# Kernel optimization log

Measured on AMD Instinct MI355X. Metric: run time of the kernel, lower is better.

Reference implementation:

```python
import jax, jax.numpy as jnp
import numpy as np

HEADS = 4
OUT_DIM = 64
NEG_SLOPE = 0.2


def setup_inputs() -> dict:
    key = jax.random.key(0)
    k1, k2, k3, k4 = jax.random.split(key, 4)
    n, in_dim = 4096, 256
    x = jax.random.normal(k1, (n, in_dim), dtype=jnp.float32)
    adj = jax.random.randint(k2, (n, n), 0, 2, dtype=jnp.int32)
    # lin: in_dim -> heads*out_dim (no bias), stored as [in_dim, heads*out_dim]
    W = jax.random.normal(k3, (in_dim, HEADS * OUT_DIM), dtype=jnp.float32) * 0.05
    # att_weight: [heads, 2*out_dim]
    att = jax.random.normal(k4, (HEADS, 2 * OUT_DIM), dtype=jnp.float32) * 0.05
    return {"x": x, "adj": adj, "W": W, "att": att}


def reference(x, adj, W, att):
    n = x.shape[0]
    h = (x @ W).reshape(n, HEADS, OUT_DIM)  # [n, H, D]
    # scores[i,j,h] = att[h] . cat(h_i, h_j) = <h_i, a_src[h]> + <h_j, a_dst[h]>
    a_src, a_dst = att[:, :OUT_DIM], att[:, OUT_DIM:]
    e_src = jnp.einsum('nhd,hd->nh', h, a_src)  # [n, H]
    e_dst = jnp.einsum('nhd,hd->nh', h, a_dst)  # [n, H]
    scores = e_src[:, None, :] + e_dst[None, :, :]  # [n, n, H]
    scores = jax.nn.leaky_relu(scores, negative_slope=NEG_SLOPE)
    mask = (adj > 0)[:, :, None]  # [n, n, 1]
    scores = jnp.where(mask, scores, -jnp.inf)
    alpha = jax.nn.softmax(scores, axis=1)  # softmax over neighbors j
    # h_prime[i,h,d] = sum_j alpha[i,j,h] * h[j,h,d]
    h_prime = jnp.einsum('ijh,jhd->ihd', alpha, h)
    return h_prime.reshape(n, HEADS * OUT_DIM)
```

## Files before the change

### kernel.cpp

```cpp
#include <hip/hip_runtime.h>
#include <hip/hip_bf16.h>

#define HEADS 4
#define ODIM 64
#define HD 256
#define NEG_SLOPE 0.2f
#define SPLITS 4
#define BJ 128

typedef __attribute__((ext_vector_type(8))) short bf16x8;
typedef __attribute__((ext_vector_type(4))) float floatx4;
typedef __attribute__((ext_vector_type(2))) float floatx2;

__global__ __launch_bounds__(256) void pack_xw(const float* __restrict__ x,
                                               const float* __restrict__ W,
                                               const int* __restrict__ adj,
                                               __hip_bfloat16* __restrict__ xh,
                                               __hip_bfloat16* __restrict__ xl,
                                               __hip_bfloat16* __restrict__ wh,
                                               __hip_bfloat16* __restrict__ wl,
                                               unsigned long long* __restrict__ adjP,
                                               int K, int n, int nxb, int nwb) {
    const int b = blockIdx.x;
    const int Kc = K >> 5;
    if (b < nxb) {
        const int g = b * 256 + threadIdx.x;
        const int lane = g & 63, frag = g >> 6;
        const int kc = frag % Kc, mc = frag / Kc;
        const int l16 = lane & 15, q = lane >> 4;
        const float* src = x + (size_t)(mc * 16 + l16) * K + kc * 32 + q * 8;
        const float4 v0 = *(const float4*)src;
        const float4 v1 = *(const float4*)(src + 4);
        const float vv[8] = {v0.x, v0.y, v0.z, v0.w, v1.x, v1.y, v1.z, v1.w};
        union { __hip_bfloat16 b[8]; bf16x8 v; } H, L;
        #pragma unroll
        for (int p = 0; p < 8; ++p) {
            H.b[p] = __float2bfloat16(vv[p]);
            L.b[p] = __float2bfloat16(vv[p] - __bfloat162float(H.b[p]));
        }
        *(bf16x8*)&xh[(size_t)frag * 512 + lane * 8] = H.v;
        *(bf16x8*)&xl[(size_t)frag * 512 + lane * 8] = L.v;
    } else if (b < nxb + nwb) {
        const int g = (b - nxb) * 256 + threadIdx.x;
        const int lane = g & 63, frag = g >> 6;
        const int kc = frag % Kc, nc = frag / Kc;
        const int l16 = lane & 15, q = lane >> 4;
        union { __hip_bfloat16 b[8]; bf16x8 v; } H, L;
        #pragma unroll
        for (int p = 0; p < 8; ++p) {
            const float w = W[(size_t)(kc * 32 + q * 8 + p) * HD + nc * 16 + l16];
            H.b[p] = __float2bfloat16(w);
            L.b[p] = __float2bfloat16(w - __bfloat162float(H.b[p]));
        }
        *(bf16x8*)&wh[(size_t)frag * 512 + lane * 8] = H.v;
        *(bf16x8*)&wl[(size_t)frag * 512 + lane * 8] = L.v;
    } else {
        const int bb = b - nxb - nwb;
        const int wv = threadIdx.x >> 6, ln = threadIdx.x & 63;
        const int gw = bb * 4 + wv;
        const int segs = n >> 6;
        for (int t = gw; t < n * 4; t += 1024) {
            const int row = t >> 2, qq = t & 3;
            const int* ar = adj + (size_t)row * n + (size_t)qq * 16 * 64;
            unsigned long long* dst = adjP + (size_t)row * segs + qq * 16;
            int v[16];
            #pragma unroll
            for (int s = 0; s < 16; ++s) v[s] = ar[s * 64 + ln];
            #pragma unroll
            for (int s = 0; s < 16; ++s) {
                const unsigned long long m = __ballot(v[s] > 0);
                if (ln == 0) dst[s] = m;
            }
        }
    }
}

__global__ __launch_bounds__(128) void gemm_fused(
    const __hip_bfloat16* __restrict__ xh, const __hip_bfloat16* __restrict__ xl,
    const __hip_bfloat16* __restrict__ wh, const __hip_bfloat16* __restrict__ wl,
    const float* __restrict__ att, float2* __restrict__ Es, float2* __restrict__ Ed,
    __hip_bfloat16* __restrict__ hbB, int n, int K) {

    __shared__ __hip_bfloat16 T[64][40];

    const int tid = threadIdx.x, wave = tid >> 6, lane = tid & 63;
    const int q = lane >> 4, l16 = lane & 15;
    const int m0 = blockIdx.x * 32;
    const int head = blockIdx.y;
    const int Kc = K >> 5;
    const int mc = (m0 >> 4) + wave;

    floatx4 acc[4] = {{0.f,0.f,0.f,0.f},{0.f,0.f,0.f,0.f},{0.f,0.f,0.f,0.f},{0.f,0.f,0.f,0.f}};

    const __hip_bfloat16* Axh = xh + (size_t)mc * Kc * 512 + lane * 8;
    const __hip_bfloat16* Axl = xl + (size_t)mc * Kc * 512 + lane * 8;
    const __hip_bfloat16* Bwh = wh + lane * 8;
    const __hip_bfloat16* Bwl = wl + lane * 8;
    #pragma unroll 2
    for (int kc = 0; kc < Kc; ++kc) {
        const bf16x8 ah = *(const bf16x8*)(Axh + (size_t)kc * 512);
        const bf16x8 al = *(const bf16x8*)(Axl + (size_t)kc * 512);
        bf16x8 bh[4], bl[4];
        #pragma unroll
        for (int nt = 0; nt < 4; ++nt) {
            const size_t fo = (size_t)((head * 4 + nt) * Kc + kc) * 512;
            bh[nt] = *(const bf16x8*)(Bwh + fo);
            bl[nt] = *(const bf16x8*)(Bwl + fo);
        }
        #pragma unroll
        for (int nt = 0; nt < 4; ++nt)
            acc[nt] = __builtin_amdgcn_mfma_f32_16x16x32_bf16(ah, bh[nt], acc[nt], 0, 0, 0);
        #pragma unroll
        for (int nt = 0; nt < 4; ++nt)
            acc[nt] = __builtin_amdgcn_mfma_f32_16x16x32_bf16(ah, bl[nt], acc[nt], 0, 0, 0);
        #pragma unroll
        for (int nt = 0; nt < 4; ++nt)
            acc[nt] = __builtin_amdgcn_mfma_f32_16x16x32_bf16(al, bh[nt], acc[nt], 0, 0, 0);
    }

    float as_v[4], ad_v[4];
    #pragma unroll
    for (int nt = 0; nt < 4; ++nt) {
        as_v[nt] = att[head * 2 * ODIM + nt * 16 + l16];
        ad_v[nt] = att[head * 2 * ODIM + ODIM + nt * 16 + l16];
    }
    #pragma unroll
    for (int r = 0; r < 4; ++r) {
        float ps = 0.f, pd = 0.f;
        #pragma unroll
        for (int nt = 0; nt < 4; ++nt) {
            ps = fmaf(acc[nt][r], as_v[nt], ps);
            pd = fmaf(acc[nt][r], ad_v[nt], pd);
        }
        #pragma unroll
        for (int m = 1; m <= 8; m <<= 1) {
            ps += __shfl_xor(ps, m, 64);
            pd += __shfl_xor(pd, m, 64);
        }
        if (l16 == 0) {
            const int i = m0 + wave * 16 + q * 4 + r;
            Es[head * n + i] = make_float2(__expf(ps), __expf(NEG_SLOPE * ps));
            Ed[head * n + i] = make_float2(__expf(pd), __expf(NEG_SLOPE * pd));
        }
    }

    #pragma unroll
    for (int nt = 0; nt < 4; ++nt) {
        union { __hip_bfloat16 b[4]; uint2 u; } pk;
        #pragma unroll
        for (int r = 0; r < 4; ++r) pk.b[r] = __float2bfloat16(acc[nt][r]);
        *(uint2*)&T[nt * 16 + l16][wave * 16 + q * 4] = pk.u;
    }
    __syncthreads();

    #pragma unroll
    for (int ffi = 0; ffi < 2; ++ffi) {
        const int f = wave + ffi * 2;
        const bf16x8 v = *(const bf16x8*)&T[f * 16 + l16][q * 8];
        const size_t frag = ((size_t)head * (n >> 5) + (m0 >> 5)) * 4 + f;
        *(bf16x8*)&hbB[frag * 512 + lane * 8] = v;
    }
}

__global__ __launch_bounds__(256, 3) void aggregate(
    const unsigned int* __restrict__ adjP32, const float2* __restrict__ Es,
    const float2* __restrict__ Ed, const __hip_bfloat16* __restrict__ hbB,
    float* __restrict__ outsp, float* __restrict__ densp, int n, int KR) {

    const int tid = threadIdx.x;
    const int wave = tid >> 6, lane = tid & 63;
    const int q = lane >> 4, l16 = lane & 15, q8 = q * 8;
    const int i0 = blockIdx.x * 32;
    const int K0 = blockIdx.y * KR;

    floatx2 es12[2];
    #pragma unroll
    for (int mt = 0; mt < 2; ++mt) {
        const float2 e = Es[(size_t)wave * n + i0 + mt * 16 + l16];
        es12[mt][0] = e.x; es12[mt][1] = e.y;
    }

    union { short s[8]; bf16x8 v; } bones;
    #pragma unroll
    for (int p = 0; p < 8; ++p) bones.s[p] = (l16 == 0) ? (short)0x3F80 : (short)0;

    floatx4 acc[2][4];
    floatx4 accd[2];
    #pragma unroll
    for (int mt = 0; mt < 2; ++mt) {
        accd[mt] = (floatx4){0.f, 0.f, 0.f, 0.f};
        #pragma unroll
        for (int nt = 0; nt < 4; ++nt) acc[mt][nt] = (floatx4){0.f, 0.f, 0.f, 0.f};
    }

    const unsigned int* aR0 = adjP32 + (size_t)(i0 + l16) * (n >> 5);
    const unsigned int* aR1 = adjP32 + (size_t)(i0 + 16 + l16) * (n >> 5);
    const float2* edp = Ed + (size_t)wave * n;
    const __hip_bfloat16* hb = hbB + ((size_t)wave * (n >> 5) * 4) * 512 + lane * 8;

    const int ksBase = K0 >> 5;
    const int nks = KR >> 5;
    const int NG = nks >> 2;

    float4 edb[2][4];
    bf16x8 hbb[2][4];
    auto ldks = [&](int s, int b) {
        const float4* ev = (const float4*)(edp + (size_t)s * 32 + q8);
        #pragma unroll
        for (int p = 0; p < 4; ++p) edb[b][p] = ev[p];
        #pragma unroll
        for (int nt = 0; nt < 4; ++nt)
            hbb[b][nt] = *(const bf16x8*)(hb + (size_t)(s * 4 + nt) * 512);
    };

    ldks(ksBase, 0);
    uint4 a0c = *(const uint4*)&aR0[ksBase];
    uint4 a1c = *(const uint4*)&aR1[ksBase];

    for (int g = 0; g < NG; ++g) {
        const int gn = (g + 1 < NG) ? g + 1 : 0;
        const uint4 a0n = *(const uint4*)&aR0[ksBase + gn * 4];
        const uint4 a1n = *(const uint4*)&aR1[ksBase + gn * 4];
        #pragma unroll
        for (int k4 = 0; k4 < 4; ++k4) {
            const int s = ksBase + g * 4 + k4;
            const int sn = (g * 4 + k4 + 1 < nks) ? s + 1 : ksBase;
            ldks(sn, (k4 + 1) & 1);
            const int cb = k4 & 1;
            const unsigned int w0 = k4 == 0 ? a0c.x : k4 == 1 ? a0c.y : k4 == 2 ? a0c.z : a0c.w;
            const unsigned int w1 = k4 == 0 ? a1c.x : k4 == 1 ? a1c.y : k4 == 2 ? a1c.z : a1c.w;
            #pragma unroll
            for (int mt = 0; mt < 2; ++mt) {
                const unsigned int wmt = mt ? w1 : w0;
                union { unsigned int u[4]; bf16x8 v; } af;
                #pragma unroll
                for (int p = 0; p < 4; ++p) {
                    const float4 e = edb[cb][p];
                    const float wa = fmaxf(es12[mt][0] * e.x, es12[mt][1] * e.y);
                    const float wb = fmaxf(es12[mt][0] * e.z, es12[mt][1] * e.w);
                    const unsigned int sh = wmt >> (q8 + 2 * p);
                    const unsigned int mm = ((sh & 1u) ? 0xFFFFu : 0u) |
                                            ((sh & 2u) ? 0xFFFF0000u : 0u);
                    af.u[p] = __builtin_amdgcn_perm(__float_as_uint(wb), __float_as_uint(wa),
                                                    0x07060302u) & mm;
                }
                #pragma unroll
                for (int nt = 0; nt < 4; ++nt)
                    acc[mt][nt] = __builtin_amdgcn_mfma_f32_16x16x32_bf16(af.v, hbb[cb][nt], acc[mt][nt], 0, 0, 0);
                accd[mt] = __builtin_amdgcn_mfma_f32_16x16x32_bf16(af.v, bones.v, accd[mt], 0, 0, 0);
            }
        }
        a0c = a0n; a1c = a1n;
    }

    const size_t sOut = (size_t)blockIdx.y * n * HD;
    #pragma unroll
    for (int mt = 0; mt < 2; ++mt)
        #pragma unroll
        for (int nt = 0; nt < 4; ++nt)
            #pragma unroll
            for (int r = 0; r < 4; ++r)
                outsp[sOut + (size_t)(i0 + mt * 16 + q * 4 + r) * HD + wave * ODIM + nt * 16 + l16] = acc[mt][nt][r];
    if (l16 == 0) {
        #pragma unroll
        for (int mt = 0; mt < 2; ++mt)
            #pragma unroll
            for (int r = 0; r < 4; ++r)
                densp[((size_t)blockIdx.y * n + i0 + mt * 16 + q * 4 + r) * HEADS + wave] = accd[mt][r];
    }
}

__global__ __launch_bounds__(256) void normalize(const float* __restrict__ outsp,
                                                 const float* __restrict__ densp,
                                                 float* __restrict__ out, int n, int splits) {
    const int g = blockIdx.x * 256 + threadIdx.x;
    const int i = g >> 6;
    const int c4 = (g & 63) * 4;
    const int head = c4 >> 6;
    float den = 0.f;
    for (int s = 0; s < splits; ++s) den += densp[((size_t)s * n + i) * HEADS + head];
    float4 v = {0.f, 0.f, 0.f, 0.f};
    for (int s = 0; s < splits; ++s) {
        const float4 t = *(const float4*)&outsp[(size_t)s * n * HD + (size_t)i * HD + c4];
        v.x += t.x; v.y += t.y; v.z += t.z; v.w += t.w;
    }
    const float inv = 1.0f / den;
    v.x *= inv; v.y *= inv; v.z *= inv; v.w *= inv;
    *(float4*)&out[(size_t)i * HD + c4] = v;
}

extern "C" void kernel_launch(void* const* d_in, const int* in_sizes, int n_in,
                              void* d_out, int out_size, void* d_ws, size_t ws_size,
                              hipStream_t stream) {
    const float* x   = (const float*)d_in[0];
    const int*   adj = (const int*)d_in[1];
    const float* W   = (const float*)d_in[2];
    const float* att = (const float*)d_in[3];
    float* out = (float*)d_out;

    const int in_dim = in_sizes[2] / HD;
    const int n = in_sizes[0] / in_dim;

    char* ws = (char*)d_ws;
    size_t off = 0;
    auto alloc = [&](size_t bytes) -> void* {
        void* p = ws + off; off += (bytes + 255) & ~(size_t)255; return p;
    };
    __hip_bfloat16* xh = (__hip_bfloat16*)alloc((size_t)n * in_dim * 2);
    __hip_bfloat16* xl = (__hip_bfloat16*)alloc((size_t)n * in_dim * 2);
    __hip_bfloat16* wh = (__hip_bfloat16*)alloc((size_t)in_dim * HD * 2);
    __hip_bfloat16* wl = (__hip_bfloat16*)alloc((size_t)in_dim * HD * 2);
    float2*         Es = (float2*)alloc((size_t)HEADS * n * 8);
    float2*         Ed = (float2*)alloc((size_t)HEADS * n * 8);
    __hip_bfloat16* hbB = (__hip_bfloat16*)alloc((size_t)n * HD * 2);
    unsigned long long* adjP = (unsigned long long*)alloc((size_t)n * (n >> 6) * 8);

    const size_t outB = (size_t)n * HD * 4, denB = (size_t)n * HEADS * 4;
    float* densp = (float*)alloc((size_t)SPLITS * denB);
    float* outsp = (float*)alloc((size_t)SPLITS * outB);

    const int nxb = (n / 16) * (in_dim / 32) * 64 / 256;
    const int nwb = (HD / 16) * (in_dim / 32) * 64 / 256;
    const int nab = 256;
    pack_xw<<<nxb + nwb + nab, 256, 0, stream>>>(x, W, adj, xh, xl, wh, wl, adjP, in_dim, n, nxb, nwb);
    gemm_fused<<<dim3(n / 32, HEADS), 128, 0, stream>>>(xh, xl, wh, wl, att, Es, Ed, hbB, n, in_dim);
    aggregate<<<dim3(n / 32, SPLITS), 256, 0, stream>>>((const unsigned int*)adjP, Es, Ed, hbB, outsp, densp, n, n / SPLITS);
    normalize<<<n * 64 / 256, 256, 0, stream>>>(outsp, densp, out, n, SPLITS);
}
```

Baseline: 167.1 us.

## Move adjacency packing into GEMM launch and enlarge aggregate row tile to 64

```diff
diff --git a/kernel.cpp b/kernel.cpp
--- a/kernel.cpp
+++ b/kernel.cpp
@@ -5,8 +5,7 @@
 #define ODIM 64
 #define HD 256
 #define NEG_SLOPE 0.2f
-#define SPLITS 4
-#define BJ 128
+#define SPLITS 8
 
 typedef __attribute__((ext_vector_type(8))) short bf16x8;
 typedef __attribute__((ext_vector_type(4))) float floatx4;
@@ -14,13 +13,11 @@
 
 __global__ __launch_bounds__(256) void pack_xw(const float* __restrict__ x,
                                                const float* __restrict__ W,
-                                               const int* __restrict__ adj,
                                                __hip_bfloat16* __restrict__ xh,
                                                __hip_bfloat16* __restrict__ xl,
                                                __hip_bfloat16* __restrict__ wh,
                                                __hip_bfloat16* __restrict__ wl,
-                                               unsigned long long* __restrict__ adjP,
-                                               int K, int n, int nxb, int nwb) {
+                                               int K, int nxb) {
     const int b = blockIdx.x;
     const int Kc = K >> 5;
     if (b < nxb) {
@@ -40,7 +37,7 @@
         }
         *(bf16x8*)&xh[(size_t)frag * 512 + lane * 8] = H.v;
         *(bf16x8*)&xl[(size_t)frag * 512 + lane * 8] = L.v;
-    } else if (b < nxb + nwb) {
+    } else {
         const int g = (b - nxb) * 256 + threadIdx.x;
         const int lane = g & 63, frag = g >> 6;
         const int kc = frag % Kc, nc = frag / Kc;
@@ -54,14 +51,27 @@
         }
         *(bf16x8*)&wh[(size_t)frag * 512 + lane * 8] = H.v;
         *(bf16x8*)&wl[(size_t)frag * 512 + lane * 8] = L.v;
-    } else {
-        const int bb = b - nxb - nwb;
+    }
+}
+
+__global__ __launch_bounds__(128) void gemm_fused(
+    const __hip_bfloat16* __restrict__ xh, const __hip_bfloat16* __restrict__ xl,
+    const __hip_bfloat16* __restrict__ wh, const __hip_bfloat16* __restrict__ wl,
+    const float* __restrict__ att, const int* __restrict__ adj,
+    float2* __restrict__ Es, float2* __restrict__ Ed,
+    __hip_bfloat16* __restrict__ hbB, unsigned long long* __restrict__ adjP,
+    int n, int K) {
+
+    __shared__ __hip_bfloat16 T[64][40];
+
+    if (blockIdx.y >= HEADS) {
+        const int bb = blockIdx.x + (blockIdx.y - HEADS) * (n >> 5);
         const int wv = threadIdx.x >> 6, ln = threadIdx.x & 63;
-        const int gw = bb * 4 + wv;
+        const int gw = bb * 2 + wv;
         const int segs = n >> 6;
-        for (int t = gw; t < n * 4; t += 1024) {
+        for (int t = gw; t < n * 4; t += 512) {
             const int row = t >> 2, qq = t & 3;
-            const int* ar = adj + (size_t)row * n + (size_t)qq * 16 * 64;
+            const int* ar = adj + (size_t)row * n + (size_t)qq * 1024;
             unsigned long long* dst = adjP + (size_t)row * segs + qq * 16;
             int v[16];
             #pragma unroll
@@ -72,16 +82,8 @@
                 if (ln == 0) dst[s] = m;
             }
         }
-    }
-}
-
-__global__ __launch_bounds__(128) void gemm_fused(
-    const __hip_bfloat16* __restrict__ xh, const __hip_bfloat16* __restrict__ xl,
-    const __hip_bfloat16* __restrict__ wh, const __hip_bfloat16* __restrict__ wl,
-    const float* __restrict__ att, float2* __restrict__ Es, float2* __restrict__ Ed,
-    __hip_bfloat16* __restrict__ hbB, int n, int K) {
-
-    __shared__ __hip_bfloat16 T[64][40];
+        return;
+    }
 
     const int tid = threadIdx.x, wave = tid >> 6, lane = tid & 63;
     const int q = lane >> 4, l16 = lane & 15;
@@ -162,7 +164,7 @@
     }
 }
 
-__global__ __launch_bounds__(256, 3) void aggregate(
+__global__ __launch_bounds__(256, 2) void aggregate(
     const unsigned int* __restrict__ adjP32, const float2* __restrict__ Es,
     const float2* __restrict__ Ed, const __hip_bfloat16* __restrict__ hbB,
     float* __restrict__ outsp, float* __restrict__ densp, int n, int KR) {
@@ -170,12 +172,12 @@
     const int tid = threadIdx.x;
     const int wave = tid >> 6, lane = tid & 63;
     const int q = lane >> 4, l16 = lane & 15, q8 = q * 8;
-    const int i0 = blockIdx.x * 32;
+    const int i0 = blockIdx.x * 64;
     const int K0 = blockIdx.y * KR;
 
-    floatx2 es12[2];
-    #pragma unroll
-    for (int mt = 0; mt < 2; ++mt) {
+    floatx2 es12[4];
+    #pragma unroll
+    for (int mt = 0; mt < 4; ++mt) {
         const float2 e = Es[(size_t)wave * n + i0 + mt * 16 + l16];
         es12[mt][0] = e.x; es12[mt][1] = e.y;
     }
@@ -184,17 +186,19 @@
     #pragma unroll
     for (int p = 0; p < 8; ++p) bones.s[p] = (l16 == 0) ? (short)0x3F80 : (short)0;
 
-    floatx4 acc[2][4];
-    floatx4 accd[2];
-    #pragma unroll
-    for (int mt = 0; mt < 2; ++mt) {
+    floatx4 acc[4][4];
+    floatx4 accd[4];
+    #pragma unroll
+    for (int mt = 0; mt < 4; ++mt) {
         accd[mt] = (floatx4){0.f, 0.f, 0.f, 0.f};
         #pragma unroll
         for (int nt = 0; nt < 4; ++nt) acc[mt][nt] = (floatx4){0.f, 0.f, 0.f, 0.f};
     }
 
-    const unsigned int* aR0 = adjP32 + (size_t)(i0 + l16) * (n >> 5);
+    const unsigned int* aR0 = adjP32 + (size_t)(i0 +      l16) * (n >> 5);
     const unsigned int* aR1 = adjP32 + (size_t)(i0 + 16 + l16) * (n >> 5);
+    const unsigned int* aR2 = adjP32 + (size_t)(i0 + 32 + l16) * (n >> 5);
+    const unsigned int* aR3 = adjP32 + (size_t)(i0 + 48 + l16) * (n >> 5);
     const float2* edp = Ed + (size_t)wave * n;
     const __hip_bfloat16* hb = hbB + ((size_t)wave * (n >> 5) * 4) * 512 + lane * 8;
 
@@ -214,24 +218,27 @@
     };
 
     ldks(ksBase, 0);
-    uint4 a0c = *(const uint4*)&aR0[ksBase];
-    uint4 a1c = *(const uint4*)&aR1[ksBase];
+    ldks(ksBase + 1, 1);
+    uint4 am0 = *(const uint4*)&aR0[ksBase];
+    uint4 am1 = *(const uint4*)&aR1[ksBase];
+    uint4 am2 = *(const uint4*)&aR2[ksBase];
+    uint4 am3 = *(const uint4*)&aR3[ksBase];
 
     for (int g = 0; g < NG; ++g) {
         const int gn = (g + 1 < NG) ? g + 1 : 0;
-        const uint4 a0n = *(const uint4*)&aR0[ksBase + gn * 4];
-        const uint4 a1n = *(const uint4*)&aR1[ksBase + gn * 4];
+        const uint4 an0 = *(const uint4*)&aR0[ksBase + gn * 4];
+        const uint4 an1 = *(const uint4*)&aR1[ksBase + gn * 4];
+        const uint4 an2 = *(const uint4*)&aR2[ksBase + gn * 4];
+        const uint4 an3 = *(const uint4*)&aR3[ksBase + gn * 4];
         #pragma unroll
         for (int k4 = 0; k4 < 4; ++k4) {
-            const int s = ksBase + g * 4 + k4;
-            const int sn = (g * 4 + k4 + 1 < nks) ? s + 1 : ksBase;
-            ldks(sn, (k4 + 1) & 1);
-            const int cb = k4 & 1;
-            const unsigned int w0 = k4 == 0 ? a0c.x : k4 == 1 ? a0c.y : k4 == 2 ? a0c.z : a0c.w;
-            const unsigned int w1 = k4 == 0 ? a1c.x : k4 == 1 ? a1c.y : k4 == 2 ? a1c.z : a1c.w;
-            #pragma unroll
-            for (int mt = 0; mt < 2; ++mt) {
-                const unsigned int wmt = mt ? w1 : w0;
+            const int sidx = g * 4 + k4;
+            const int cb = sidx & 1;
+            #pragma unroll
+            for (int mt = 0; mt < 4; ++mt) {
+                const uint4 amv = mt == 0 ? am0 : mt == 1 ? am1 : mt == 2 ? am2 : am3;
+                const unsigned int wmt = k4 == 0 ? amv.x : k4 == 1 ? amv.y
+                                       : k4 == 2 ? amv.z : amv.w;
                 union { unsigned int u[4]; bf16x8 v; } af;
                 #pragma unroll
                 for (int p = 0; p < 4; ++p) {
@@ -249,13 +256,15 @@
                     acc[mt][nt] = __builtin_amdgcn_mfma_f32_16x16x32_bf16(af.v, hbb[cb][nt], acc[mt][nt], 0, 0, 0);
                 accd[mt] = __builtin_amdgcn_mfma_f32_16x16x32_bf16(af.v, bones.v, accd[mt], 0, 0, 0);
             }
-        }
-        a0c = a0n; a1c = a1n;
+            const int sn2 = (sidx + 2 < nks) ? ksBase + sidx + 2 : ksBase;
+            ldks(sn2, cb);
+        }
+        am0 = an0; am1 = an1; am2 = an2; am3 = an3;
     }
 
     const size_t sOut = (size_t)blockIdx.y * n * HD;
     #pragma unroll
-    for (int mt = 0; mt < 2; ++mt)
+    for (int mt = 0; mt < 4; ++mt)
         #pragma unroll
         for (int nt = 0; nt < 4; ++nt)
             #pragma unroll
@@ -263,7 +272,7 @@
                 outsp[sOut + (size_t)(i0 + mt * 16 + q * 4 + r) * HD + wave * ODIM + nt * 16 + l16] = acc[mt][nt][r];
     if (l16 == 0) {
         #pragma unroll
-        for (int mt = 0; mt < 2; ++mt)
+        for (int mt = 0; mt < 4; ++mt)
             #pragma unroll
             for (int r = 0; r < 4; ++r)
                 densp[((size_t)blockIdx.y * n + i0 + mt * 16 + q * 4 + r) * HEADS + wave] = accd[mt][r];
@@ -316,14 +325,18 @@
     unsigned long long* adjP = (unsigned long long*)alloc((size_t)n * (n >> 6) * 8);
 
     const size_t outB = (size_t)n * HD * 4, denB = (size_t)n * HEADS * 4;
-    float* densp = (float*)alloc((size_t)SPLITS * denB);
-    float* outsp = (float*)alloc((size_t)SPLITS * outB);
+    int splits = SPLITS;
+    if (ws_size && off + (size_t)splits * (((outB + 255) & ~(size_t)255) + ((denB + 255) & ~(size_t)255)) > ws_size)
+        splits = 4;
+    float* densp = (float*)alloc((size_t)splits * denB);
+    float* outsp = (float*)alloc((size_t)splits * outB);
 
     const int nxb = (n / 16) * (in_dim / 32) * 64 / 256;
     const int nwb = (HD / 16) * (in_dim / 32) * 64 / 256;
-    const int nab = 256;
-    pack_xw<<<nxb + nwb + nab, 256, 0, stream>>>(x, W, adj, xh, xl, wh, wl, adjP, in_dim, n, nxb, nwb);
-    gemm_fused<<<dim3(n / 32, HEADS), 128, 0, stream>>>(xh, xl, wh, wl, att, Es, Ed, hbB, n, in_dim);
-    aggregate<<<dim3(n / 32, SPLITS), 256, 0, stream>>>((const unsigned int*)adjP, Es, Ed, hbB, outsp, densp, n, n / SPLITS);
-    normalize<<<n * 64 / 256, 256, 0, stream>>>(outsp, densp, out, n, SPLITS);
-}
+    pack_xw<<<nxb + nwb, 256, 0, stream>>>(x, W, xh, xl, wh, wl, in_dim, nxb);
+    gemm_fused<<<dim3(n / 32, HEADS + 2), 128, 0, stream>>>(xh, xl, wh, wl, att, adj,
+                                                            Es, Ed, hbB, adjP, n, in_dim);
+    aggregate<<<dim3(n / 64, splits), 256, 0, stream>>>((const unsigned int*)adjP, Es, Ed,
+                                                        hbB, outsp, densp, n, n / splits);
+    normalize<<<n * 64 / 256, 256, 0, stream>>>(outsp, densp, out, n, splits);
+}
```

Measured after the change: 165.7 us. About the same (-0.8%).
